# Kernel optimization log

Measured on AMD Instinct MI355X. Metric: run time of the kernel, lower is better.

Reference implementation:

```python
import jax, jax.numpy as jnp
import numpy as np

K = 256  # number of leaf nodes in the cluster tree


def setup_inputs() -> dict:
    key = jax.random.key(0)
    k1, k2 = jax.random.split(key)
    minibatch = jax.random.normal(k1, (131072, 64), dtype=jnp.float32)
    centers = jax.random.normal(k2, (K, 64), dtype=jnp.float32)
    return {"minibatch": minibatch, "centers": centers}


def reference(minibatch, centers):
    # Euclidean cdist (p=2) between samples [N,D] and leaf centers [K,D]
    x_sq = jnp.sum(minibatch * minibatch, axis=1, keepdims=True)      # [N,1]
    c_sq = jnp.sum(centers * centers, axis=1)[None, :]                # [1,K]
    dist_sq = x_sq + c_sq - 2.0 * (minibatch @ centers.T)             # [N,K]
    dist_sq = jnp.maximum(dist_sq, 0.0)
    dist = jnp.sqrt(dist_sq)

    # nearest-leaf routing (torch.min over dim=1)
    assignments = jnp.argmin(dist, axis=1)                            # [N] int
    min_dists = jnp.min(dist, axis=1)                                 # [N]

    # per-leaf statistics (vectorized form of the per-node assignment loop):
    # counts -> node.assignments length, sums -> analytic center updates,
    # sum_sq -> node.sum_squared_dist
    ones = jnp.ones(minibatch.shape[0], dtype=minibatch.dtype)
    leaf_counts = jax.ops.segment_sum(ones, assignments, num_segments=K)           # [K]
    leaf_sums = jax.ops.segment_sum(minibatch, assignments, num_segments=K)        # [K,D]
    leaf_sum_sq_dist = jax.ops.segment_sum(min_dists * min_dists, assignments,
                                           num_segments=K)                         # [K]
    return assignments, min_dists, leaf_counts, leaf_sums, leaf_sum_sq_dist
```

## Files before the change

kernel.cpp:

```cpp
#include <hip/hip_runtime.h>
#include <hip/hip_bf16.h>
#include <float.h>

#define NS 131072
#define DD 64
#define KK 256
#define CPAD 72
#define NSTAT 16896
#define XTS 264
#define XTSW 132
#define NCOPY 512
#define RGROUPS 16
#define RPER 32
#define SCR_OFF_F ((size_t)NCOPY * NSTAT / 2)
#define P_OFF_F   (SCR_OFF_F + (size_t)RGROUPS * NSTAT)
#define P_CSQ_F 9216
#define P_IMG_I4 2304

typedef __attribute__((ext_vector_type(8))) short bf16x8;
typedef __attribute__((ext_vector_type(4))) float f32x4;
typedef __attribute__((ext_vector_type(4))) unsigned int u32x4;


__global__ void zero_buf(float* __restrict__ p, int n) {
    int i = blockIdx.x * 256 + threadIdx.x;
    if (i < n) p[i] = 0.f;
}

__device__ inline unsigned short f2bf(float f) {
    union { __hip_bfloat16 h; unsigned short u; } v;
    v.h = __float2bfloat16(f);
    return v.u;
}
__device__ inline float bf2f(unsigned short b) {
    return __uint_as_float(((unsigned)b) << 16);
}

__global__ void prep_centers(const float* __restrict__ ctr, float* __restrict__ P) {
    __shared__ float s_part[32][9];
    const int t = threadIdx.x;
    const int rl = t >> 3, seg = t & 7;
    const int r = blockIdx.x * 32 + rl;
    const float* rp = ctr + r * DD + seg * 8;
    float4 a = ((const float4*)rp)[0];
    float4 b = ((const float4*)rp)[1];
    unsigned short u0 = f2bf(a.x), u1 = f2bf(a.y), u2 = f2bf(a.z), u3 = f2bf(a.w);
    unsigned short u4 = f2bf(b.x), u5 = f2bf(b.y), u6 = f2bf(b.z), u7 = f2bf(b.w);
    float q0 = bf2f(u0), q1 = bf2f(u1), q2 = bf2f(u2), q3 = bf2f(u3);
    float q4 = bf2f(u4), q5 = bf2f(u5), q6 = bf2f(u6), q7 = bf2f(u7);
    float p = (q0*q0 + q1*q1 + q2*q2 + q3*q3) + (q4*q4 + q5*q5 + q6*q6 + q7*q7);

    unsigned short* Pu = (unsigned short*)P;
    int4 pack;
    pack.x = (int)((unsigned)u0 | ((unsigned)u1 << 16));
    pack.y = (int)((unsigned)u2 | ((unsigned)u3 << 16));
    pack.z = (int)((unsigned)u4 | ((unsigned)u5 << 16));
    pack.w = (int)((unsigned)u6 | ((unsigned)u7 << 16));
    *(int4*)(Pu + (size_t)r * CPAD + seg * 8) = pack;
    if (seg == 0) {
        int4 z; z.x = 0; z.y = 0; z.z = 0; z.w = 0;
        *(int4*)(Pu + (size_t)r * CPAD + 64) = z;
    }
    s_part[rl][seg] = p;
    __syncthreads();
    if (seg == 0) {
        float s = 0.f;
        #pragma unroll
        for (int k = 0; k < 8; ++k) s += s_part[rl][k];
        P[P_CSQ_F + r] = s;
    }
}

__global__ __launch_bounds__(256, 4)
void deepect_argmin(const float* __restrict__ mb, const float* __restrict__ P,
                    float* __restrict__ out) {
    __shared__ __align__(16) unsigned short s_ctr[KK][CPAD];
    __shared__ float s_csq[KK];

    const int tid  = threadIdx.x;
    const int lane = tid & 63;
    const int w    = tid >> 6;
    const int g    = lane >> 4;
    const int c16  = lane & 15;

    {
        const int4* Pi = (const int4*)P;
        int4* Sd = (int4*)s_ctr;
        #pragma unroll
        for (int i = 0; i < 9; ++i)
            Sd[i * 256 + tid] = Pi[i * 256 + tid];
    }
    s_csq[tid] = P[P_CSQ_F + tid];
    __syncthreads();

    float csqh[16];
    #pragma unroll
    for (int t = 0; t < 16; ++t) csqh[t] = -0.5f * s_csq[t * 16 + c16];

    const int sbase = blockIdx.x * 128 + w * 32;

    bf16x8 afr[2][2];
    float  xsq_rt[2];
    #pragma unroll
    for (int rt = 0; rt < 2; ++rt) {
        float px = 0.f;
        #pragma unroll
        for (int ks = 0; ks < 2; ++ks) {
            const float* rp = mb + (size_t)(sbase + rt * 16 + c16) * DD + g * 8 + ks * 32;
            float4 a = ((const float4*)rp)[0];
            float4 b = ((const float4*)rp)[1];
            bf16x8 f;
            f[0] = (short)f2bf(a.x); f[1] = (short)f2bf(a.y);
            f[2] = (short)f2bf(a.z); f[3] = (short)f2bf(a.w);
            f[4] = (short)f2bf(b.x); f[5] = (short)f2bf(b.y);
            f[6] = (short)f2bf(b.z); f[7] = (short)f2bf(b.w);
            afr[rt][ks] = f;
            px += a.x*a.x + a.y*a.y + a.z*a.z + a.w*a.w
                + b.x*b.x + b.y*b.y + b.z*b.z + b.w*b.w;
        }
        px += __shfl_xor(px, 16, 64);
        px += __shfl_xor(px, 32, 64);
        xsq_rt[rt] = px;
    }

    float bestv[2][4];
    int   besti[2][4];
    #pragma unroll
    for (int rt = 0; rt < 2; ++rt)
        #pragma unroll
        for (int r = 0; r < 4; ++r) { bestv[rt][r] = -FLT_MAX; besti[rt][r] = 0; }

    #pragma unroll
    for (int t = 0; t < 16; ++t) {
        const bf16x8 b0 = *(const bf16x8*)&s_ctr[t * 16 + c16][g * 8];
        const bf16x8 b1 = *(const bf16x8*)&s_ctr[t * 16 + c16][g * 8 + 32];
        const int colidx = t * 16 + c16;
        #pragma unroll
        for (int rt = 0; rt < 2; ++rt) {
            f32x4 acc;
            acc[0] = csqh[t]; acc[1] = csqh[t]; acc[2] = csqh[t]; acc[3] = csqh[t];
            acc = __builtin_amdgcn_mfma_f32_16x16x32_bf16(afr[rt][0], b0, acc, 0, 0, 0);
            acc = __builtin_amdgcn_mfma_f32_16x16x32_bf16(afr[rt][1], b1, acc, 0, 0, 0);
            #pragma unroll
            for (int r = 0; r < 4; ++r) {
                if (acc[r] > bestv[rt][r]) { bestv[rt][r] = acc[r]; besti[rt][r] = colidx; }
            }
        }
    }

    float* o_assign = out;
    float* o_mind   = out + NS;

    #pragma unroll
    for (int rt = 0; rt < 2; ++rt) {
        #pragma unroll
        for (int r = 0; r < 4; ++r) {
            float v  = bestv[rt][r];
            int   bi = besti[rt][r];
            #pragma unroll
            for (int off = 1; off < 16; off <<= 1) {
                float ov = __shfl_xor(v, off, 64);
                int   oi = __shfl_xor(bi, off, 64);
                if (ov > v || (ov == v && oi < bi)) { v = ov; bi = oi; }
            }
            int src = (lane & 48) | (g * 4 + r);
            float xq = __shfl(xsq_rt[rt], src, 64);
            float dsq = fmaxf(xq - 2.0f * v, 0.f);
            if (c16 == 0) {
                int s = sbase + rt * 16 + g * 4 + r;
                o_assign[s] = (float)bi;
                o_mind[s]   = sqrtf(dsq);
            }
        }
    }
}

__global__ __launch_bounds__(512, 2)
void deepect_stats_gemm(const float* __restrict__ mb, const float* __restrict__ out,
                        float* __restrict__ ws) {
    __shared__ __align__(16) unsigned short s_xt[80][XTS];
    __shared__ int s_bi[256];

    const int tid  = threadIdx.x;
    const int lane = tid & 63;
    const int w    = tid >> 6;
    const int g    = lane >> 4;
    const int c16  = lane & 15;
    const int base = blockIdx.x * 256;

    unsigned* xtw = (unsigned*)s_xt;

    for (int i = tid; i < 14 * XTSW; i += 512) xtw[66 * XTSW + i] = 0u;

    {
        const int dh = tid >> 7, sp = tid & 127;
        const float* r0 = mb + (size_t)(base + 2 * sp) * DD + dh * 16;
        const float* r1 = r0 + DD;
        #pragma unroll
        for (int q = 0; q < 4; ++q) {
            float4 a = ((const float4*)r0)[q];
            float4 b = ((const float4*)r1)[q];
            const int row = dh * 16 + q * 4;
            xtw[(row + 0) * XTSW + sp] = (unsigned)f2bf(a.x) | ((unsigned)f2bf(b.x) << 16);
            xtw[(row + 1) * XTSW + sp] = (unsigned)f2bf(a.y) | ((unsigned)f2bf(b.y) << 16);
            xtw[(row + 2) * XTSW + sp] = (unsigned)f2bf(a.z) | ((unsigned)f2bf(b.z) << 16);
            xtw[(row + 3) * XTSW + sp] = (unsigned)f2bf(a.w) | ((unsigned)f2bf(b.w) << 16);
        }
    }
    if (tid < 128) {
        const int sp = tid;
        float m0 = out[NS + base + 2 * sp];
        float m1 = out[NS + base + 2 * sp + 1];
        xtw[64 * XTSW + sp] = 0x3F803F80u;
        xtw[65 * XTSW + sp] = (unsigned)f2bf(m0 * m0) | ((unsigned)f2bf(m1 * m1) << 16);
    }
    if (tid < 256) s_bi[tid] = (int)out[base + tid];
    __syncthreads();

    f32x4 acc[2][5];
    #pragma unroll
    for (int L = 0; L < 2; ++L)
        #pragma unroll
        for (int dt = 0; dt < 5; ++dt) {
            acc[L][dt][0] = 0.f; acc[L][dt][1] = 0.f;
            acc[L][dt][2] = 0.f; acc[L][dt][3] = 0.f;
        }

    const int ml0 = w * 16 + c16;
    const int ml1 = (w + 8) * 16 + c16;

    #pragma unroll
    for (int ks = 0; ks < 8; ++ks) {
        const int kb = ks * 32 + g * 8;
        int4 bl = *(int4*)&s_bi[kb];
        int4 bh = *(int4*)&s_bi[kb + 4];
        bf16x8 bfrag[5];
        #pragma unroll
        for (int dt = 0; dt < 5; ++dt)
            bfrag[dt] = *(bf16x8*)&s_xt[dt * 16 + c16][kb];

        const int b0 = bl.x, b1 = bl.y, b2 = bl.z, b3 = bl.w;
        const int b4 = bh.x, b5 = bh.y, b6 = bh.z, b7 = bh.w;
        u32x4 u0, u1;
        u0[0] = (b0 == ml0 ? 0x3F80u : 0u) | (b1 == ml0 ? 0x3F800000u : 0u);
        u0[1] = (b2 == ml0 ? 0x3F80u : 0u) | (b3 == ml0 ? 0x3F800000u : 0u);
        u0[2] = (b4 == ml0 ? 0x3F80u : 0u) | (b5 == ml0 ? 0x3F800000u : 0u);
        u0[3] = (b6 == ml0 ? 0x3F80u : 0u) | (b7 == ml0 ? 0x3F800000u : 0u);
        u1[0] = (b0 == ml1 ? 0x3F80u : 0u) | (b1 == ml1 ? 0x3F800000u : 0u);
        u1[1] = (b2 == ml1 ? 0x3F80u : 0u) | (b3 == ml1 ? 0x3F800000u : 0u);
        u1[2] = (b4 == ml1 ? 0x3F80u : 0u) | (b5 == ml1 ? 0x3F800000u : 0u);
        u1[3] = (b6 == ml1 ? 0x3F80u : 0u) | (b7 == ml1 ? 0x3F800000u : 0u);
        bf16x8 a0 = __builtin_bit_cast(bf16x8, u0);
        bf16x8 a1 = __builtin_bit_cast(bf16x8, u1);

        #pragma unroll
        for (int dt = 0; dt < 5; ++dt) {
            acc[0][dt] = __builtin_amdgcn_mfma_f32_16x16x32_bf16(a0, bfrag[dt], acc[0][dt], 0, 0, 0);
            acc[1][dt] = __builtin_amdgcn_mfma_f32_16x16x32_bf16(a1, bfrag[dt], acc[1][dt], 0, 0, 0);
        }
    }

    unsigned short* dstu = (unsigned short*)ws + (size_t)blockIdx.x * NSTAT;
    #pragma unroll
    for (int L = 0; L < 2; ++L) {
        const int lt = (L == 0) ? w : (w + 8);
        #pragma unroll
        for (int dt = 0; dt < 5; ++dt) {
            const int col = dt * 16 + c16;
            #pragma unroll
            for (int r = 0; r < 4; ++r) {
                const int leaf = lt * 16 + g * 4 + r;
                if (col < 66) dstu[leaf * 66 + col] = f2bf(acc[L][dt][r]);
            }
        }
    }
}

__global__ void reduce_ws1(float* __restrict__ ws) {
    int gid = blockIdx.x * 256 + threadIdx.x;
    if (gid >= NSTAT * RGROUPS) return;
    int g = gid / NSTAT, e = gid - g * NSTAT;
    const unsigned short* src = (const unsigned short*)ws + (size_t)(g * RPER) * NSTAT + e;
    float s = 0.f;
    #pragma unroll 8
    for (int j = 0; j < RPER; ++j) s += bf2f(src[(size_t)j * NSTAT]);
    ws[SCR_OFF_F + (size_t)g * NSTAT + e] = s;
}

__global__ void reduce_ws2(const float* __restrict__ ws, float* __restrict__ o_stats) {
    int e = blockIdx.x * 256 + threadIdx.x;
    if (e >= NSTAT) return;
    float s = 0.f;
    #pragma unroll
    for (int g = 0; g < RGROUPS; ++g) s += ws[SCR_OFF_F + (size_t)g * NSTAT + e];
    int leaf = e / 66, c = e - leaf * 66;
    float* o_cnt = o_stats;
    float* o_sum = o_stats + KK;
    float* o_ssq = o_stats + KK + KK * DD;
    if (c < 64)       o_sum[leaf * 64 + c] = s;
    else if (c == 64) o_cnt[leaf] = s;
    else              o_ssq[leaf] = s;
}

__global__ __launch_bounds__(512, 2)
void deepect_argmin_fb(const float* __restrict__ mb, const float* __restrict__ ctr,
                       float* __restrict__ out) {
    __shared__ __align__(16) unsigned short s_ctr[KK][CPAD];
    __shared__ float s_csq[KK];

    const int tid  = threadIdx.x;
    const int lane = tid & 63;
    const int w    = tid >> 6;
    const int g    = lane >> 4;
    const int c16  = lane & 15;

    for (int idx = tid; idx < KK * 16; idx += 512) {
        int row = idx >> 4, f4 = idx & 15;
        float4 v = ((const float4*)(ctr + row * DD))[f4];
        ushort4 b;
        b.x = f2bf(v.x); b.y = f2bf(v.y); b.z = f2bf(v.z); b.w = f2bf(v.w);
        *(ushort4*)&s_ctr[row][f4 * 4] = b;
    }
    __syncthreads();

    if (tid < KK) {
        float acc = 0.f;
        #pragma unroll
        for (int j = 0; j < 16; ++j) {
            ushort4 b = *(ushort4*)&s_ctr[tid][j * 4];
            float x0 = bf2f(b.x), x1 = bf2f(b.y), x2 = bf2f(b.z), x3 = bf2f(b.w);
            acc += x0 * x0 + x1 * x1 + x2 * x2 + x3 * x3;
        }
        s_csq[tid] = acc;
    }
    __syncthreads();

    float csqh[16];
    #pragma unroll
    for (int t = 0; t < 16; ++t) csqh[t] = -0.5f * s_csq[t * 16 + c16];

    const int sbase = blockIdx.x * 256 + w * 32;

    bf16x8 afr[2][2];
    float  xsq_rt[2];
    #pragma unroll
    for (int rt = 0; rt < 2; ++rt) {
        float px = 0.f;
        #pragma unroll
        for (int ks = 0; ks < 2; ++ks) {
            const float* rp = mb + (size_t)(sbase + rt * 16 + c16) * DD + g * 8 + ks * 32;
            float4 a = ((const float4*)rp)[0];
            float4 b = ((const float4*)rp)[1];
            bf16x8 f;
            f[0] = (short)f2bf(a.x); f[1] = (short)f2bf(a.y);
            f[2] = (short)f2bf(a.z); f[3] = (short)f2bf(a.w);
            f[4] = (short)f2bf(b.x); f[5] = (short)f2bf(b.y);
            f[6] = (short)f2bf(b.z); f[7] = (short)f2bf(b.w);
            afr[rt][ks] = f;
            px += a.x*a.x + a.y*a.y + a.z*a.z + a.w*a.w
                + b.x*b.x + b.y*b.y + b.z*b.z + b.w*b.w;
        }
        px += __shfl_xor(px, 16, 64);
        px += __shfl_xor(px, 32, 64);
        xsq_rt[rt] = px;
    }

    float bestv[2][4];
    int   besti[2][4];
    #pragma unroll
    for (int rt = 0; rt < 2; ++rt)
        #pragma unroll
        for (int r = 0; r < 4; ++r) { bestv[rt][r] = -FLT_MAX; besti[rt][r] = 0; }

    #pragma unroll
    for (int t = 0; t < 16; ++t) {
        bf16x8 b0 = *(bf16x8*)&s_ctr[t * 16 + c16][g * 8];
        bf16x8 b1 = *(bf16x8*)&s_ctr[t * 16 + c16][g * 8 + 32];
        const int colidx = t * 16 + c16;
        #pragma unroll
        for (int rt = 0; rt < 2; ++rt) {
            f32x4 acc;
            acc[0] = csqh[t]; acc[1] = csqh[t]; acc[2] = csqh[t]; acc[3] = csqh[t];
            acc = __builtin_amdgcn_mfma_f32_16x16x32_bf16(afr[rt][0], b0, acc, 0, 0, 0);
            acc = __builtin_amdgcn_mfma_f32_16x16x32_bf16(afr[rt][1], b1, acc, 0, 0, 0);
            #pragma unroll
            for (int r = 0; r < 4; ++r) {
                if (acc[r] > bestv[rt][r]) { bestv[rt][r] = acc[r]; besti[rt][r] = colidx; }
            }
        }
    }

    float* o_assign = out;
    float* o_mind   = out + NS;

    #pragma unroll
    for (int rt = 0; rt < 2; ++rt) {
        #pragma unroll
        for (int r = 0; r < 4; ++r) {
            float v  = bestv[rt][r];
            int   bi = besti[rt][r];
            #pragma unroll
            for (int off = 1; off < 16; off <<= 1) {
                float ov = __shfl_xor(v, off, 64);
                int   oi = __shfl_xor(bi, off, 64);
                if (ov > v || (ov == v && oi < bi)) { v = ov; bi = oi; }
            }
            int src = (lane & 48) | (g * 4 + r);
            float xq = __shfl(xsq_rt[rt], src, 64);
            float dsq = fmaxf(xq - 2.0f * v, 0.f);
            if (c16 == 0) {
                int s = sbase + rt * 16 + g * 4 + r;
                o_assign[s] = (float)bi;
                o_mind[s]   = sqrtf(dsq);
            }
        }
    }
}

__global__ __launch_bounds__(512)
void deepect_stats_atomic(const float* __restrict__ mb, const float* __restrict__ out,
                          float* __restrict__ o_stats) {
    __shared__ float s_cnt[KK];
    __shared__ float s_ssq[KK];
    __shared__ float s_sum[KK][65];

    const int tid = threadIdx.x;
    for (int idx = tid; idx < KK; idx += 512) { s_cnt[idx] = 0.f; s_ssq[idx] = 0.f; }
    for (int idx = tid; idx < KK * 65; idx += 512) ((float*)s_sum)[idx] = 0.f;
    __syncthreads();

    const int grp = tid >> 4;
    const int d4  = tid & 15;
    const int ibase = blockIdx.x * 512 + grp * 16;

    for (int s = 0; s < 16; ++s) {
        const int i = ibase + s;
        const int bi = (int)out[i];
        float4 v = ((const float4*)(mb + (size_t)i * DD))[d4];
        atomicAdd(&s_sum[bi][d4 * 4 + 0], v.x);
        atomicAdd(&s_sum[bi][d4 * 4 + 1], v.y);
        atomicAdd(&s_sum[bi][d4 * 4 + 2], v.z);
        atomicAdd(&s_sum[bi][d4 * 4 + 3], v.w);
        if (d4 == 0) {
            const float md = out[NS + i];
            atomicAdd(&s_cnt[bi], 1.0f);
            atomicAdd(&s_ssq[bi], md * md);
        }
    }
    __syncthreads();

    for (int idx = tid; idx < KK; idx += 512) {
        atomicAdd(&o_stats[idx], s_cnt[idx]);
        atomicAdd(&o_stats[KK + KK * DD + idx], s_ssq[idx]);
    }
    for (int idx = tid; idx < KK * DD; idx += 512)
        atomicAdd(&o_stats[KK + idx], s_sum[idx >> 6][idx & 63]);
}

extern "C" void kernel_launch(void* const* d_in, const int* in_sizes, int n_in,
                              void* d_out, int out_size, void* d_ws, size_t ws_size,
                              hipStream_t stream) {
    const float* mb  = (const float*)d_in[0];
    const float* ctr = (const float*)d_in[1];
    float* out = (float*)d_out;
    float* o_stats = out + 2 * NS;
    float* ws = (float*)d_ws;

    const size_t need = (P_OFF_F + P_CSQ_F + KK) * sizeof(float);

    if (ws_size >= need) {
        float* P = ws + P_OFF_F;
        hipLaunchKernelGGL(prep_centers, dim3(8), dim3(256), 0, stream, ctr, P);
        hipLaunchKernelGGL(deepect_argmin, dim3(NS / 128), dim3(256), 0, stream,
                           mb, P, out);
        hipLaunchKernelGGL(deepect_stats_gemm, dim3(NS / 256), dim3(512), 0, stream,
                           mb, out, ws);
        hipLaunchKernelGGL(reduce_ws1, dim3((NSTAT * RGROUPS + 255) / 256), dim3(256),
                           0, stream, ws);
        hipLaunchKernelGGL(reduce_ws2, dim3((NSTAT + 255) / 256), dim3(256), 0, stream,
                           ws, o_stats);
    } else {
        hipLaunchKernelGGL(zero_buf, dim3((NSTAT + 255) / 256), dim3(256), 0, stream,
                           o_stats, NSTAT);
        hipLaunchKernelGGL(deepect_argmin_fb, dim3(NS / 256), dim3(512), 0, stream,
                           mb, ctr, out);
        hipLaunchKernelGGL(deepect_stats_atomic, dim3(NS / 512), dim3(512), 0, stream,
                           mb, out, o_stats);
    }
}
```

Measured before the change: 58.45 us.

## Stage centers through half-size LDS buffer in two phases to double occupancy

The argmin kernel now keeps only 128 center rows in LDS at a time. It loads the first half, runs MFMAs over centers 0-127, syncs, reloads the second half and processes centers 128-255, with launch bounds raised from 4 to 8 blocks per CU. Sample loading is also moved ahead of the center load so the global reads can overlap. The aim is more resident waves to hide latency, at the cost of two extra barriers and reloading centers from global/L2 per half.

```diff
diff --git a/kernel.cpp b/kernel.cpp
--- a/kernel.cpp
+++ b/kernel.cpp
@@ -16,6 +16,7 @@
 #define P_OFF_F   (SCR_OFF_F + (size_t)RGROUPS * NSTAT)
 #define P_CSQ_F 9216
 #define P_IMG_I4 2304
+#define P_HALF_I4 1152
 
 typedef __attribute__((ext_vector_type(8))) short bf16x8;
 typedef __attribute__((ext_vector_type(4))) float f32x4;
@@ -71,10 +72,10 @@
     }
 }
 
-__global__ __launch_bounds__(256, 4)
+__global__ __launch_bounds__(256, 8)
 void deepect_argmin(const float* __restrict__ mb, const float* __restrict__ P,
                     float* __restrict__ out) {
-    __shared__ __align__(16) unsigned short s_ctr[KK][CPAD];
+    __shared__ __align__(16) unsigned short s_ctr[128][CPAD];
     __shared__ float s_csq[KK];
 
     const int tid  = threadIdx.x;
@@ -83,21 +84,9 @@
     const int g    = lane >> 4;
     const int c16  = lane & 15;
 
-    {
-        const int4* Pi = (const int4*)P;
-        int4* Sd = (int4*)s_ctr;
-        #pragma unroll
-        for (int i = 0; i < 9; ++i)
-            Sd[i * 256 + tid] = Pi[i * 256 + tid];
-    }
-    s_csq[tid] = P[P_CSQ_F + tid];
-    __syncthreads();
-
-    float csqh[16];
-    #pragma unroll
-    for (int t = 0; t < 16; ++t) csqh[t] = -0.5f * s_csq[t * 16 + c16];
-
     const int sbase = blockIdx.x * 128 + w * 32;
+    const int4* Pi = (const int4*)P;
+    int4* Sd = (int4*)s_ctr;
 
     bf16x8 afr[2][2];
     float  xsq_rt[2];
@@ -123,6 +112,18 @@
         xsq_rt[rt] = px;
     }
 
+    #pragma unroll
+    for (int i = 0; i < 5; ++i) {
+        int idx = i * 256 + tid;
+        if (idx < P_HALF_I4) Sd[idx] = Pi[idx];
+    }
+    s_csq[tid] = P[P_CSQ_F + tid];
+    __syncthreads();
+
+    float csqh[16];
+    #pragma unroll
+    for (int t = 0; t < 16; ++t) csqh[t] = -0.5f * s_csq[t * 16 + c16];
+
     float bestv[2][4];
     int   besti[2][4];
     #pragma unroll
@@ -131,9 +132,35 @@
         for (int r = 0; r < 4; ++r) { bestv[rt][r] = -FLT_MAX; besti[rt][r] = 0; }
 
     #pragma unroll
-    for (int t = 0; t < 16; ++t) {
+    for (int t = 0; t < 8; ++t) {
         const bf16x8 b0 = *(const bf16x8*)&s_ctr[t * 16 + c16][g * 8];
         const bf16x8 b1 = *(const bf16x8*)&s_ctr[t * 16 + c16][g * 8 + 32];
+        const int colidx = t * 16 + c16;
+        #pragma unroll
+        for (int rt = 0; rt < 2; ++rt) {
+            f32x4 acc;
+            acc[0] = csqh[t]; acc[1] = csqh[t]; acc[2] = csqh[t]; acc[3] = csqh[t];
+            acc = __builtin_amdgcn_mfma_f32_16x16x32_bf16(afr[rt][0], b0, acc, 0, 0, 0);
+            acc = __builtin_amdgcn_mfma_f32_16x16x32_bf16(afr[rt][1], b1, acc, 0, 0, 0);
+            #pragma unroll
+            for (int r = 0; r < 4; ++r) {
+                if (acc[r] > bestv[rt][r]) { bestv[rt][r] = acc[r]; besti[rt][r] = colidx; }
+            }
+        }
+    }
+    __syncthreads();
+
+    #pragma unroll
+    for (int i = 0; i < 5; ++i) {
+        int idx = i * 256 + tid;
+        if (idx < P_HALF_I4) Sd[idx] = Pi[P_HALF_I4 + idx];
+    }
+    __syncthreads();
+
+    #pragma unroll
+    for (int t = 8; t < 16; ++t) {
+        const bf16x8 b0 = *(const bf16x8*)&s_ctr[(t - 8) * 16 + c16][g * 8];
+        const bf16x8 b1 = *(const bf16x8*)&s_ctr[(t - 8) * 16 + c16][g * 8 + 32];
         const int colidx = t * 16 + c16;
         #pragma unroll
         for (int rt = 0; rt < 2; ++rt) {
```

After: 126.5 us. +116.3%, slower.
